# Kernel optimization log

Hardware: AMD Instinct MI355X
Metric: run time of the kernel (lower is better)

Reference implementation:

```python
import jax, jax.numpy as jnp
import numpy as np


def _maxpool2x2(x):
    # x: [B, C, H, W] -> [B, C, H//2, W//2]
    B, C, H, W = x.shape
    return x.reshape(B, C, H // 2, 2, W // 2, 2).max(axis=(3, 5))


def setup_inputs() -> dict:
    key = jax.random.key(0)
    ks = jax.random.split(key, 6)
    B, CH, H, W = 16, 128, 64, 64
    W_SCALE = 0.05  # keep pre-softmax logits in a sane range
    x = jax.random.normal(ks[0], (B, CH, H, W), dtype=jnp.float32)
    w_theta = jax.random.normal(ks[1], (CH // 8, CH), dtype=jnp.float32) * W_SCALE
    w_phi = jax.random.normal(ks[2], (CH // 8, CH), dtype=jnp.float32) * W_SCALE
    w_g = jax.random.normal(ks[3], (CH // 2, CH), dtype=jnp.float32) * W_SCALE
    w_o = jax.random.normal(ks[4], (CH, CH // 2), dtype=jnp.float32) * W_SCALE
    gamma = jax.random.normal(ks[5], (1,), dtype=jnp.float32)  # torch inits to 0; randomized for non-trivial output
    return {"x": x, "w_theta": w_theta, "w_phi": w_phi, "w_g": w_g, "w_o": w_o, "gamma": gamma}


def reference(x, w_theta, w_phi, w_g, w_o, gamma):
    B, C, H, W = x.shape
    N = H * W
    # 1x1 convs are channel GEMMs
    theta = jnp.einsum('oc,bchw->bohw', w_theta, x)          # [B, C/8, H, W]
    phi = _maxpool2x2(jnp.einsum('oc,bchw->bohw', w_phi, x))  # [B, C/8, H/2, W/2]
    g = _maxpool2x2(jnp.einsum('oc,bchw->bohw', w_g, x))      # [B, C/2, H/2, W/2]
    theta = theta.reshape(B, C // 8, N)        # [B, C/8, N]
    phi = phi.reshape(B, C // 8, N // 4)       # [B, C/8, N/4]
    g = g.reshape(B, C // 2, N // 4)           # [B, C/2, N/4]
    scores = jnp.einsum('bcn,bcm->bnm', theta, phi)  # [B, N, N/4]
    beta = jax.nn.softmax(scores, axis=-1)
    o = jnp.einsum('bcm,bnm->bcn', g, beta)          # [B, C/2, N]
    o = o.reshape(B, C // 2, H, W)
    o = jnp.einsum('oc,bchw->bohw', w_o, o)          # [B, C, H, W]
    return gamma[0] * o + x
```

## Files before the change

### kernel.cpp

```cpp
#include <hip/hip_runtime.h>
#include <hip/hip_bf16.h>


typedef __attribute__((ext_vector_type(8))) short bf16x8;
typedef __attribute__((ext_vector_type(16))) float f32x16;

#define LOG2E 1.4426950408889634f

__device__ __forceinline__ ushort f2bf(float f) {
    uint u = __float_as_uint(f);
    u += 0x7FFFu + ((u >> 16) & 1u);
    return (ushort)(u >> 16);
}
__device__ __forceinline__ uint pk2(float a, float b) {
    return (uint)f2bf(a) | ((uint)f2bf(b) << 16);
}
__device__ __forceinline__ uint pk2hw(float a, float b) {
    union { __hip_bfloat162 h; uint u; } cv;
    cv.h = __float22bfloat162_rn(make_float2(a, b));
    return cv.u;
}
__device__ __forceinline__ float exp2_hw(float v) {
    float r;
    asm("v_exp_f32 %0, %1" : "=v"(r) : "v"(v));
    return r;
}

__global__ __launch_bounds__(256) void k_convs(const float* __restrict__ x,
                                               const float* __restrict__ w_theta,
                                               const float* __restrict__ w_phi,
                                               const float* __restrict__ w_g,
                                               ushort* __restrict__ theta_b,
                                               ushort* __restrict__ phi_b,
                                               ushort* __restrict__ g_b) {
    __shared__ __align__(16) char smem[16384 + 32 * 72 * 2];
    const int tid = threadIdx.x;
    const int part = blockIdx.x >> 8;
    const int pb = blockIdx.x & 255;
    const int gq = pb * 64 + (tid >> 2);
    const int sub = tid & 3;
    const int b = gq >> 10, m = gq & 1023;
    const int h2 = m >> 5, w2 = m & 31;
    const int n = (2 * h2 + (sub >> 1)) * 64 + 2 * w2 + (sub & 1);
    const float* xp = x + (size_t)b * 128 * 4096 + n;

    if (part == 0) {
        float (*wt)[32] = (float (*)[32])smem;
        for (int i = tid; i < 2048; i += 256) { int o = i >> 7, c = i & 127; wt[c][o] = w_theta[i] * LOG2E; }
        for (int i = tid; i < 2048; i += 256) { int o = i >> 7, c = i & 127; wt[c][16 + o] = w_phi[i]; }
        __syncthreads();
        float th[16], ph[16];
#pragma unroll
        for (int o = 0; o < 16; ++o) { th[o] = 0.f; ph[o] = 0.f; }
        for (int c = 0; c < 128; ++c) {
            float xv = xp[(size_t)c * 4096];
            const float* wr = wt[c];
#pragma unroll
            for (int o = 0; o < 16; ++o) th[o] = fmaf(wr[o], xv, th[o]);
#pragma unroll
            for (int o = 0; o < 16; ++o) ph[o] = fmaf(wr[16 + o], xv, ph[o]);
        }
        uint4 t0, t1;
        t0.x = pk2(th[0], th[1]);  t0.y = pk2(th[2], th[3]);
        t0.z = pk2(th[4], th[5]);  t0.w = pk2(th[6], th[7]);
        t1.x = pk2(th[8], th[9]);  t1.y = pk2(th[10], th[11]);
        t1.z = pk2(th[12], th[13]); t1.w = pk2(th[14], th[15]);
        uint4* tp = (uint4*)(theta_b + ((size_t)b * 4096 + n) * 16);
        tp[0] = t0; tp[1] = t1;
#pragma unroll
        for (int o = 0; o < 16; ++o) {
            ph[o] = fmaxf(ph[o], __shfl_xor(ph[o], 1));
            ph[o] = fmaxf(ph[o], __shfl_xor(ph[o], 2));
        }
        if (sub == 0) {
            uint4 p0, p1;
            p0.x = pk2(ph[0], ph[1]);  p0.y = pk2(ph[2], ph[3]);
            p0.z = pk2(ph[4], ph[5]);  p0.w = pk2(ph[6], ph[7]);
            p1.x = pk2(ph[8], ph[9]);  p1.y = pk2(ph[10], ph[11]);
            p1.z = pk2(ph[12], ph[13]); p1.w = pk2(ph[14], ph[15]);
            uint4* pp = (uint4*)(phi_b + ((size_t)b * 1024 + m) * 16);
            pp[0] = p0; pp[1] = p1;
        }
    } else {
        const int gp = part - 1;
        float (*wg)[32] = (float (*)[32])smem;
        ushort (*gt)[72] = (ushort (*)[72])(smem + 16384);
        for (int i = tid; i < 4096; i += 256) { int o = i >> 7, c = i & 127; wg[c][o] = w_g[(gp * 32 + o) * 128 + c]; }
        __syncthreads();
        float gg[32];
#pragma unroll
        for (int o = 0; o < 32; ++o) gg[o] = 0.f;
        for (int c = 0; c < 128; ++c) {
            float xv = xp[(size_t)c * 4096];
            const float* wr = wg[c];
#pragma unroll
            for (int o = 0; o < 32; ++o) gg[o] = fmaf(wr[o], xv, gg[o]);
        }
#pragma unroll
        for (int o = 0; o < 32; ++o) {
            gg[o] = fmaxf(gg[o], __shfl_xor(gg[o], 1));
            gg[o] = fmaxf(gg[o], __shfl_xor(gg[o], 2));
        }
        const int col = tid >> 2;
#pragma unroll
        for (int cc = 0; cc < 8; ++cc) gt[8 * sub + cc][col] = f2bf(gg[8 * sub + cc]);
        __syncthreads();
        const int cl = tid >> 3, q = tid & 7;
        uint4 v = *(const uint4*)&gt[cl][8 * q];
        const int bb = pb >> 4, mb = (pb & 15) * 64;
        *(uint4*)(g_b + ((size_t)bb * 64 + gp * 32 + cl) * 1024 + mb + 8 * q) = v;
    }
}

__global__ __launch_bounds__(256) void k_attn(const ushort* __restrict__ theta_b,
                                              const ushort* __restrict__ phi_b,
                                              const ushort* __restrict__ g_b,
                                              const float* __restrict__ w_o,
                                              const float* __restrict__ x,
                                              const float* __restrict__ gamma,
                                              float* __restrict__ out) {
    const int tid = threadIdx.x;
    const int wave = tid >> 6, lane = tid & 63;
    const int l31 = lane & 31, h = lane >> 5;
    const int b = blockIdx.x >> 5, nt = blockIdx.x & 31;
    const int n = nt * 128 + wave * 32 + l31;

    bf16x8 thf = *(const bf16x8*)(theta_b + ((size_t)b * 4096 + n) * 16 + h * 8);

    const ushort* pbase = phi_b + (size_t)b * 1024 * 16 + h * 8;
    const ushort* gbase = g_b + ((size_t)b * 64 + l31) * 1024 + 8 * h;

    f32x16 o0 = {0,0,0,0,0,0,0,0,0,0,0,0,0,0,0,0};
    f32x16 o1 = {0,0,0,0,0,0,0,0,0,0,0,0,0,0,0,0};
    float sm0 = 0.f, sm1 = 0.f;

    bf16x8 phf = *(const bf16x8*)(pbase + (size_t)l31 * 16);
    bf16x8 gA0 = *(const bf16x8*)(gbase);
    bf16x8 gA1 = *(const bf16x8*)(gbase + 32 * 1024);
    bf16x8 gB0 = *(const bf16x8*)(gbase + 16);
    bf16x8 gB1 = *(const bf16x8*)(gbase + 16 + 32 * 1024);

    for (int mt = 0; mt < 32; ++mt) {
        const int m1 = ((mt + 1) & 31) * 32;
        bf16x8 nphf = *(const bf16x8*)(pbase + (size_t)(m1 + l31) * 16);
        bf16x8 ngA0 = *(const bf16x8*)(gbase + m1);
        bf16x8 ngA1 = *(const bf16x8*)(gbase + m1 + 32 * 1024);
        bf16x8 ngB0 = *(const bf16x8*)(gbase + m1 + 16);
        bf16x8 ngB1 = *(const bf16x8*)(gbase + m1 + 16 + 32 * 1024);

        f32x16 S = {0,0,0,0,0,0,0,0,0,0,0,0,0,0,0,0};
        S = __builtin_amdgcn_mfma_f32_32x32x16_bf16(phf, thf, S, 0, 0, 0);
        float p[16];
#pragma unroll
        for (int jj = 0; jj < 16; ++jj) p[jj] = exp2_hw(S[jj]);
        sm0 += ((p[0] + p[1]) + (p[2] + p[3])) + ((p[4] + p[5]) + (p[6] + p[7]));
        sm1 += ((p[8] + p[9]) + (p[10] + p[11])) + ((p[12] + p[13]) + (p[14] + p[15]));

        uint c0 = pk2hw(p[0], p[1]),   c1 = pk2hw(p[2], p[3]);
        uint c2 = pk2hw(p[4], p[5]),   c3 = pk2hw(p[6], p[7]);
        uint c4 = pk2hw(p[8], p[9]),   c5 = pk2hw(p[10], p[11]);
        uint c6 = pk2hw(p[12], p[13]), c7 = pk2hw(p[14], p[15]);
        uint q0 = (uint)__shfl_xor((int)(h ? c0 : c2), 32);
        uint q1 = (uint)__shfl_xor((int)(h ? c1 : c3), 32);
        uint q2 = (uint)__shfl_xor((int)(h ? c4 : c6), 32);
        uint q3 = (uint)__shfl_xor((int)(h ? c5 : c7), 32);
        union { bf16x8 v; uint u[4]; } B0, B1;
        if (h == 0) {
            B0.u[0] = c0; B0.u[1] = c1; B0.u[2] = q0; B0.u[3] = q1;
            B1.u[0] = c4; B1.u[1] = c5; B1.u[2] = q2; B1.u[3] = q3;
        } else {
            B0.u[0] = q0; B0.u[1] = q1; B0.u[2] = c2; B0.u[3] = c3;
            B1.u[0] = q2; B1.u[1] = q3; B1.u[2] = c6; B1.u[3] = c7;
        }
        o0 = __builtin_amdgcn_mfma_f32_32x32x16_bf16(gA0, B0.v, o0, 0, 0, 0);
        o1 = __builtin_amdgcn_mfma_f32_32x32x16_bf16(gA1, B0.v, o1, 0, 0, 0);
        o0 = __builtin_amdgcn_mfma_f32_32x32x16_bf16(gB0, B1.v, o0, 0, 0, 0);
        o1 = __builtin_amdgcn_mfma_f32_32x32x16_bf16(gB1, B1.v, o1, 0, 0, 0);

        phf = nphf; gA0 = ngA0; gA1 = ngA1; gB0 = ngB0; gB1 = ngB1;
    }
    float sm = sm0 + sm1;
    sm += __shfl_xor(sm, 32);
    const float inv = 1.f / sm;
#pragma unroll
    for (int jj = 0; jj < 16; ++jj) { o0[jj] *= inv; o1[jj] *= inv; }

    bf16x8 Bf[4];
#pragma unroll
    for (int kc = 0; kc < 4; ++kc) {
        const f32x16& oo = (kc < 2) ? o0 : o1;
        const int base = 8 * (kc & 1);
        uint Pa0 = pk2(oo[base + 0], oo[base + 1]);
        uint Pa1 = pk2(oo[base + 2], oo[base + 3]);
        uint Pb0 = pk2(oo[base + 4], oo[base + 5]);
        uint Pb1 = pk2(oo[base + 6], oo[base + 7]);
        uint z0 = h ? Pa0 : Pb0, z1 = h ? Pa1 : Pb1;
        uint r0 = (uint)__shfl_xor((int)z0, 32);
        uint r1 = (uint)__shfl_xor((int)z1, 32);
        union { bf16x8 v; uint u[4]; } Bx;
        if (h == 0) { Bx.u[0] = Pa0; Bx.u[1] = Pa1; Bx.u[2] = r0;  Bx.u[3] = r1; }
        else        { Bx.u[0] = r0;  Bx.u[1] = r1;  Bx.u[2] = Pb0; Bx.u[3] = Pb1; }
        Bf[kc] = Bx.v;
    }

    const float gm = gamma[0];
#pragma unroll
    for (int cof = 0; cof < 4; ++cof) {
        f32x16 oc = {0,0,0,0,0,0,0,0,0,0,0,0,0,0,0,0};
#pragma unroll
        for (int kc = 0; kc < 4; ++kc) {
            const float* wp = w_o + (32 * cof + l31) * 64 + 16 * kc + 8 * h;
            float4 wa = *(const float4*)(wp);
            float4 wb = *(const float4*)(wp + 4);
            union { bf16x8 v; uint u[4]; } W;
            W.u[0] = pk2(wa.x, wa.y); W.u[1] = pk2(wa.z, wa.w);
            W.u[2] = pk2(wb.x, wb.y); W.u[3] = pk2(wb.z, wb.w);
            oc = __builtin_amdgcn_mfma_f32_32x32x16_bf16(W.v, Bf[kc], oc, 0, 0, 0);
        }
#pragma unroll
        for (int jj = 0; jj < 16; ++jj) {
            int co = 32 * cof + (jj & 3) + 8 * (jj >> 2) + 4 * h;
            size_t idx = ((size_t)(b * 128 + co)) * 4096 + n;
            out[idx] = fmaf(gm, oc[jj], x[idx]);
        }
    }
}

extern "C" void kernel_launch(void* const* d_in, const int* in_sizes, int n_in,
                              void* d_out, int out_size, void* d_ws, size_t ws_size,
                              hipStream_t stream) {
    const float* x       = (const float*)d_in[0];
    const float* w_theta = (const float*)d_in[1];
    const float* w_phi   = (const float*)d_in[2];
    const float* w_g     = (const float*)d_in[3];
    const float* w_o     = (const float*)d_in[4];
    const float* gamma   = (const float*)d_in[5];
    float* out = (float*)d_out;

    ushort* theta_b = (ushort*)d_ws;
    ushort* phi_b   = theta_b + 1048576;
    ushort* g_b     = phi_b + 262144;

    k_convs<<<768, 256, 0, stream>>>(x, w_theta, w_phi, w_g, theta_b, phi_b, g_b);
    k_attn<<<512, 256, 0, stream>>>(theta_b, phi_b, g_b, w_o, x, gamma, out);
}
```

Baseline: 162.5 us.

## Use MFMA for projection convs and stage phi/g tiles through LDS in attention

The conv kernel is rewritten so each block stages a bf16, XOR-swizzled x tile and packed bf16 weight fragments in LDS, then computes theta, phi and g with MFMA instead of scalar FMA loops. It also fuses all three projections into one block type, cutting the grid from 768 to 512 blocks and removing the redundant reads of x across parts. The attention kernel now loads phi/g fragments cooperatively into a double-buffered LDS ring shared across the four waves, instead of each wave fetching them from global memory. The cost is bf16 rounding of x and the weights before the projections, more LDS use, and a block barrier per group of four key tiles.

After: 146.1 us. -10.1%, faster.

```diff
diff --git a/kernel.cpp b/kernel.cpp
--- a/kernel.cpp
+++ b/kernel.cpp
@@ -33,82 +33,115 @@
                                                ushort* __restrict__ theta_b,
                                                ushort* __restrict__ phi_b,
                                                ushort* __restrict__ g_b) {
-    __shared__ __align__(16) char smem[16384 + 32 * 72 * 2];
+    __shared__ uint  xl[8192];
+    __shared__ uint4 wl[1536];
     const int tid = threadIdx.x;
-    const int part = blockIdx.x >> 8;
-    const int pb = blockIdx.x & 255;
-    const int gq = pb * 64 + (tid >> 2);
-    const int sub = tid & 3;
-    const int b = gq >> 10, m = gq & 1023;
-    const int h2 = m >> 5, w2 = m & 31;
-    const int n = (2 * h2 + (sub >> 1)) * 64 + 2 * w2 + (sub & 1);
-    const float* xp = x + (size_t)b * 128 * 4096 + n;
-
-    if (part == 0) {
-        float (*wt)[32] = (float (*)[32])smem;
-        for (int i = tid; i < 2048; i += 256) { int o = i >> 7, c = i & 127; wt[c][o] = w_theta[i] * LOG2E; }
-        for (int i = tid; i < 2048; i += 256) { int o = i >> 7, c = i & 127; wt[c][16 + o] = w_phi[i]; }
-        __syncthreads();
-        float th[16], ph[16];
-#pragma unroll
-        for (int o = 0; o < 16; ++o) { th[o] = 0.f; ph[o] = 0.f; }
-        for (int c = 0; c < 128; ++c) {
-            float xv = xp[(size_t)c * 4096];
-            const float* wr = wt[c];
-#pragma unroll
-            for (int o = 0; o < 16; ++o) th[o] = fmaf(wr[o], xv, th[o]);
-#pragma unroll
-            for (int o = 0; o < 16; ++o) ph[o] = fmaf(wr[16 + o], xv, ph[o]);
-        }
-        uint4 t0, t1;
-        t0.x = pk2(th[0], th[1]);  t0.y = pk2(th[2], th[3]);
-        t0.z = pk2(th[4], th[5]);  t0.w = pk2(th[6], th[7]);
-        t1.x = pk2(th[8], th[9]);  t1.y = pk2(th[10], th[11]);
-        t1.z = pk2(th[12], th[13]); t1.w = pk2(th[14], th[15]);
-        uint4* tp = (uint4*)(theta_b + ((size_t)b * 4096 + n) * 16);
-        tp[0] = t0; tp[1] = t1;
-#pragma unroll
-        for (int o = 0; o < 16; ++o) {
-            ph[o] = fmaxf(ph[o], __shfl_xor(ph[o], 1));
-            ph[o] = fmaxf(ph[o], __shfl_xor(ph[o], 2));
-        }
-        if (sub == 0) {
-            uint4 p0, p1;
-            p0.x = pk2(ph[0], ph[1]);  p0.y = pk2(ph[2], ph[3]);
-            p0.z = pk2(ph[4], ph[5]);  p0.w = pk2(ph[6], ph[7]);
-            p1.x = pk2(ph[8], ph[9]);  p1.y = pk2(ph[10], ph[11]);
-            p1.z = pk2(ph[12], ph[13]); p1.w = pk2(ph[14], ph[15]);
-            uint4* pp = (uint4*)(phi_b + ((size_t)b * 1024 + m) * 16);
-            pp[0] = p0; pp[1] = p1;
-        }
-    } else {
-        const int gp = part - 1;
-        float (*wg)[32] = (float (*)[32])smem;
-        ushort (*gt)[72] = (ushort (*)[72])(smem + 16384);
-        for (int i = tid; i < 4096; i += 256) { int o = i >> 7, c = i & 127; wg[c][o] = w_g[(gp * 32 + o) * 128 + c]; }
-        __syncthreads();
-        float gg[32];
-#pragma unroll
-        for (int o = 0; o < 32; ++o) gg[o] = 0.f;
-        for (int c = 0; c < 128; ++c) {
-            float xv = xp[(size_t)c * 4096];
-            const float* wr = wg[c];
-#pragma unroll
-            for (int o = 0; o < 32; ++o) gg[o] = fmaf(wr[o], xv, gg[o]);
-        }
-#pragma unroll
-        for (int o = 0; o < 32; ++o) {
-            gg[o] = fmaxf(gg[o], __shfl_xor(gg[o], 1));
-            gg[o] = fmaxf(gg[o], __shfl_xor(gg[o], 2));
-        }
-        const int col = tid >> 2;
-#pragma unroll
-        for (int cc = 0; cc < 8; ++cc) gt[8 * sub + cc][col] = f2bf(gg[8 * sub + cc]);
-        __syncthreads();
-        const int cl = tid >> 3, q = tid & 7;
-        uint4 v = *(const uint4*)&gt[cl][8 * q];
-        const int bb = pb >> 4, mb = (pb & 15) * 64;
-        *(uint4*)(g_b + ((size_t)bb * 64 + gp * 32 + cl) * 1024 + mb + 8 * q) = v;
+    const int b = blockIdx.x >> 5, h2 = blockIdx.x & 31;
+    const int p0 = h2 * 128;
+
+    {
+        const int cp = tid & 63, pg = tid >> 6;
+        const float* r0 = x + ((size_t)(b * 128 + 2 * cp)) * 4096 + p0 + pg * 32;
+        const float4* v0 = (const float4*)r0;
+        const float4* v1 = (const float4*)(r0 + 4096);
+#pragma unroll
+        for (int j = 0; j < 8; ++j) {
+            float4 a = v0[j], c = v1[j];
+            const float* af = (const float*)&a;
+            const float* cf = (const float*)&c;
+#pragma unroll
+            for (int e = 0; e < 4; ++e) {
+                int pix = pg * 32 + 4 * j + e;
+                uint u = pk2hw(af[e], cf[e]);
+                int byt = (pix * 256 + cp * 4) ^ ((pix & 15) << 4);
+                xl[byt >> 2] = u;
+            }
+        }
+    }
+#pragma unroll
+    for (int i = 0; i < 6; ++i) {
+        int fi = tid + 256 * i;
+        int ln = fi & 63, sk = fi >> 6;
+        int s = sk >> 3, kc = sk & 7;
+        int r31 = ln & 31, rh = ln >> 5;
+        int c0 = kc * 16 + rh * 8;
+        const float* wr;
+        float scale = 1.0f;
+        if (s == 0) {
+            if (r31 < 16) { wr = w_theta + r31 * 128 + c0; scale = LOG2E; }
+            else          { wr = w_phi + (r31 - 16) * 128 + c0; }
+        } else if (s == 1) { wr = w_g + r31 * 128 + c0; }
+        else               { wr = w_g + (r31 + 32) * 128 + c0; }
+        float4 wa = *(const float4*)wr, wb = *(const float4*)(wr + 4);
+        uint4 fr;
+        fr.x = pk2hw(wa.x * scale, wa.y * scale);
+        fr.y = pk2hw(wa.z * scale, wa.w * scale);
+        fr.z = pk2hw(wb.x * scale, wb.y * scale);
+        fr.w = pk2hw(wb.z * scale, wb.w * scale);
+        wl[fi] = fr;
+    }
+    __syncthreads();
+
+    const int lane = tid & 63, wv = tid >> 6;
+    const int l31 = lane & 31, hh = lane >> 5;
+    const int sub = l31 & 3, q = wv * 8 + (l31 >> 2);
+    const int pix = 64 * (sub >> 1) + 2 * q + (sub & 1);
+    f32x16 a0 = {0,0,0,0,0,0,0,0,0,0,0,0,0,0,0,0};
+    f32x16 a1 = {0,0,0,0,0,0,0,0,0,0,0,0,0,0,0,0};
+    f32x16 a2 = {0,0,0,0,0,0,0,0,0,0,0,0,0,0,0,0};
+#pragma unroll
+    for (int kc = 0; kc < 8; ++kc) {
+        int byt = (pix * 256 + 32 * kc + 16 * hh) ^ ((pix & 15) << 4);
+        bf16x8 xf = *(const bf16x8*)((const char*)xl + byt);
+        bf16x8 w0 = *(const bf16x8*)&wl[(0 * 8 + kc) * 64 + lane];
+        bf16x8 w1 = *(const bf16x8*)&wl[(1 * 8 + kc) * 64 + lane];
+        bf16x8 w2 = *(const bf16x8*)&wl[(2 * 8 + kc) * 64 + lane];
+        a0 = __builtin_amdgcn_mfma_f32_32x32x16_bf16(w0, xf, a0, 0, 0, 0);
+        a1 = __builtin_amdgcn_mfma_f32_32x32x16_bf16(w1, xf, a1, 0, 0, 0);
+        a2 = __builtin_amdgcn_mfma_f32_32x32x16_bf16(w2, xf, a2, 0, 0, 0);
+    }
+
+    {
+        const int n = h2 * 128 + pix;
+        ushort* tp = theta_b + ((size_t)b * 4096 + n) * 16;
+        uint2 t0, t1;
+        t0.x = pk2hw(a0[0], a0[1]); t0.y = pk2hw(a0[2], a0[3]);
+        t1.x = pk2hw(a0[4], a0[5]); t1.y = pk2hw(a0[6], a0[7]);
+        *(uint2*)(tp + 4 * hh) = t0;
+        *(uint2*)(tp + 8 + 4 * hh) = t1;
+    }
+    float ph[8], g0[16], g1[16];
+#pragma unroll
+    for (int jj = 0; jj < 8; ++jj) ph[jj] = a0[8 + jj];
+#pragma unroll
+    for (int jj = 0; jj < 16; ++jj) { g0[jj] = a1[jj]; g1[jj] = a2[jj]; }
+#pragma unroll
+    for (int jj = 0; jj < 8; ++jj) {
+        ph[jj] = fmaxf(ph[jj], __shfl_xor(ph[jj], 1));
+        ph[jj] = fmaxf(ph[jj], __shfl_xor(ph[jj], 2));
+    }
+#pragma unroll
+    for (int jj = 0; jj < 16; ++jj) {
+        g0[jj] = fmaxf(g0[jj], __shfl_xor(g0[jj], 1));
+        g0[jj] = fmaxf(g0[jj], __shfl_xor(g0[jj], 2));
+        g1[jj] = fmaxf(g1[jj], __shfl_xor(g1[jj], 1));
+        g1[jj] = fmaxf(g1[jj], __shfl_xor(g1[jj], 2));
+    }
+    if (sub == 0) {
+        const int m = h2 * 32 + q;
+        ushort* pp = phi_b + ((size_t)b * 1024 + m) * 16;
+        uint2 p0v, p1v;
+        p0v.x = pk2hw(ph[0], ph[1]); p0v.y = pk2hw(ph[2], ph[3]);
+        p1v.x = pk2hw(ph[4], ph[5]); p1v.y = pk2hw(ph[6], ph[7]);
+        *(uint2*)(pp + 4 * hh) = p0v;
+        *(uint2*)(pp + 8 + 4 * hh) = p1v;
+        ushort* gp = g_b + (size_t)b * 64 * 1024 + m;
+#pragma unroll
+        for (int jj = 0; jj < 16; ++jj) {
+            int oc = (jj & 3) + 8 * (jj >> 2) + 4 * hh;
+            gp[(size_t)oc * 1024] = f2bf(g0[jj]);
+            gp[(size_t)(oc + 32) * 1024] = f2bf(g1[jj]);
+        }
     }
 }
 
@@ -119,6 +152,7 @@
                                               const float* __restrict__ x,
                                               const float* __restrict__ gamma,
                                               float* __restrict__ out) {
+    __shared__ uint4 sbuf[2][20][64];
     const int tid = threadIdx.x;
     const int wave = tid >> 6, lane = tid & 63;
     const int l31 = lane & 31, h = lane >> 5;
@@ -127,58 +161,85 @@
 
     bf16x8 thf = *(const bf16x8*)(theta_b + ((size_t)b * 4096 + n) * 16 + h * 8);
 
-    const ushort* pbase = phi_b + (size_t)b * 1024 * 16 + h * 8;
-    const ushort* gbase = g_b + ((size_t)b * 64 + l31) * 1024 + 8 * h;
+    const ushort* sp[5];
+    int sstep[5];
+#pragma unroll
+    for (int i = 0; i < 5; ++i) {
+        int mtLf = (tid >> 6) + 4 * i;
+        int mtL = mtLf / 5, f = mtLf % 5;
+        int m0 = mtL * 32;
+        if (f == 0) {
+            sp[i] = phi_b + ((size_t)b * 1024 + m0 + l31) * 16 + 8 * h;
+            sstep[i] = 128 * 16;
+        } else {
+            int off = (f >= 3 ? 16 : 0) + ((f == 2 || f == 4) ? 32 * 1024 : 0);
+            sp[i] = g_b + ((size_t)b * 64 + l31) * 1024 + m0 + 8 * h + off;
+            sstep[i] = 128;
+        }
+    }
+
+    uint4 stg[5];
+#pragma unroll
+    for (int i = 0; i < 5; ++i) { stg[i] = *(const uint4*)sp[i]; sp[i] += sstep[i]; }
+#pragma unroll
+    for (int i = 0; i < 5; ++i) sbuf[0][(tid >> 6) + 4 * i][lane] = stg[i];
+    __syncthreads();
 
     f32x16 o0 = {0,0,0,0,0,0,0,0,0,0,0,0,0,0,0,0};
     f32x16 o1 = {0,0,0,0,0,0,0,0,0,0,0,0,0,0,0,0};
     float sm0 = 0.f, sm1 = 0.f;
 
-    bf16x8 phf = *(const bf16x8*)(pbase + (size_t)l31 * 16);
-    bf16x8 gA0 = *(const bf16x8*)(gbase);
-    bf16x8 gA1 = *(const bf16x8*)(gbase + 32 * 1024);
-    bf16x8 gB0 = *(const bf16x8*)(gbase + 16);
-    bf16x8 gB1 = *(const bf16x8*)(gbase + 16 + 32 * 1024);
-
-    for (int mt = 0; mt < 32; ++mt) {
-        const int m1 = ((mt + 1) & 31) * 32;
-        bf16x8 nphf = *(const bf16x8*)(pbase + (size_t)(m1 + l31) * 16);
-        bf16x8 ngA0 = *(const bf16x8*)(gbase + m1);
-        bf16x8 ngA1 = *(const bf16x8*)(gbase + m1 + 32 * 1024);
-        bf16x8 ngB0 = *(const bf16x8*)(gbase + m1 + 16);
-        bf16x8 ngB1 = *(const bf16x8*)(gbase + m1 + 16 + 32 * 1024);
-
-        f32x16 S = {0,0,0,0,0,0,0,0,0,0,0,0,0,0,0,0};
-        S = __builtin_amdgcn_mfma_f32_32x32x16_bf16(phf, thf, S, 0, 0, 0);
-        float p[16];
-#pragma unroll
-        for (int jj = 0; jj < 16; ++jj) p[jj] = exp2_hw(S[jj]);
-        sm0 += ((p[0] + p[1]) + (p[2] + p[3])) + ((p[4] + p[5]) + (p[6] + p[7]));
-        sm1 += ((p[8] + p[9]) + (p[10] + p[11])) + ((p[12] + p[13]) + (p[14] + p[15]));
-
-        uint c0 = pk2hw(p[0], p[1]),   c1 = pk2hw(p[2], p[3]);
-        uint c2 = pk2hw(p[4], p[5]),   c3 = pk2hw(p[6], p[7]);
-        uint c4 = pk2hw(p[8], p[9]),   c5 = pk2hw(p[10], p[11]);
-        uint c6 = pk2hw(p[12], p[13]), c7 = pk2hw(p[14], p[15]);
-        uint q0 = (uint)__shfl_xor((int)(h ? c0 : c2), 32);
-        uint q1 = (uint)__shfl_xor((int)(h ? c1 : c3), 32);
-        uint q2 = (uint)__shfl_xor((int)(h ? c4 : c6), 32);
-        uint q3 = (uint)__shfl_xor((int)(h ? c5 : c7), 32);
-        union { bf16x8 v; uint u[4]; } B0, B1;
-        if (h == 0) {
-            B0.u[0] = c0; B0.u[1] = c1; B0.u[2] = q0; B0.u[3] = q1;
-            B1.u[0] = c4; B1.u[1] = c5; B1.u[2] = q2; B1.u[3] = q3;
-        } else {
-            B0.u[0] = q0; B0.u[1] = q1; B0.u[2] = c2; B0.u[3] = c3;
-            B1.u[0] = q2; B1.u[1] = q3; B1.u[2] = c6; B1.u[3] = c7;
-        }
-        o0 = __builtin_amdgcn_mfma_f32_32x32x16_bf16(gA0, B0.v, o0, 0, 0, 0);
-        o1 = __builtin_amdgcn_mfma_f32_32x32x16_bf16(gA1, B0.v, o1, 0, 0, 0);
-        o0 = __builtin_amdgcn_mfma_f32_32x32x16_bf16(gB0, B1.v, o0, 0, 0, 0);
-        o1 = __builtin_amdgcn_mfma_f32_32x32x16_bf16(gB1, B1.v, o1, 0, 0, 0);
-
-        phf = nphf; gA0 = ngA0; gA1 = ngA1; gB0 = ngB0; gB1 = ngB1;
-    }
+    for (int grp = 0; grp < 8; ++grp) {
+        const int cur = grp & 1;
+        if (grp < 7) {
+#pragma unroll
+            for (int i = 0; i < 5; ++i) { stg[i] = *(const uint4*)sp[i]; sp[i] += sstep[i]; }
+        }
+#pragma unroll
+        for (int mtL = 0; mtL < 4; ++mtL) {
+            const uint4* fr = &sbuf[cur][mtL * 5][0];
+            bf16x8 phf = *(const bf16x8*)&fr[0 * 64 + lane];
+            bf16x8 gA0 = *(const bf16x8*)&fr[1 * 64 + lane];
+            bf16x8 gA1 = *(const bf16x8*)&fr[2 * 64 + lane];
+            bf16x8 gB0 = *(const bf16x8*)&fr[3 * 64 + lane];
+            bf16x8 gB1 = *(const bf16x8*)&fr[4 * 64 + lane];
+
+            f32x16 S = {0,0,0,0,0,0,0,0,0,0,0,0,0,0,0,0};
+            S = __builtin_amdgcn_mfma_f32_32x32x16_bf16(phf, thf, S, 0, 0, 0);
+            float p[16];
+#pragma unroll
+            for (int jj = 0; jj < 16; ++jj) p[jj] = exp2_hw(S[jj]);
+            sm0 += ((p[0] + p[1]) + (p[2] + p[3])) + ((p[4] + p[5]) + (p[6] + p[7]));
+            sm1 += ((p[8] + p[9]) + (p[10] + p[11])) + ((p[12] + p[13]) + (p[14] + p[15]));
+
+            uint c0 = pk2hw(p[0], p[1]),   c1 = pk2hw(p[2], p[3]);
+            uint c2 = pk2hw(p[4], p[5]),   c3 = pk2hw(p[6], p[7]);
+            uint c4 = pk2hw(p[8], p[9]),   c5 = pk2hw(p[10], p[11]);
+            uint c6 = pk2hw(p[12], p[13]), c7 = pk2hw(p[14], p[15]);
+            uint q0 = (uint)__shfl_xor((int)(h ? c0 : c2), 32);
+            uint q1 = (uint)__shfl_xor((int)(h ? c1 : c3), 32);
+            uint q2 = (uint)__shfl_xor((int)(h ? c4 : c6), 32);
+            uint q3 = (uint)__shfl_xor((int)(h ? c5 : c7), 32);
+            union { bf16x8 v; uint u[4]; } B0, B1;
+            if (h == 0) {
+                B0.u[0] = c0; B0.u[1] = c1; B0.u[2] = q0; B0.u[3] = q1;
+                B1.u[0] = c4; B1.u[1] = c5; B1.u[2] = q2; B1.u[3] = q3;
+            } else {
+                B0.u[0] = q0; B0.u[1] = q1; B0.u[2] = c2; B0.u[3] = c3;
+                B1.u[0] = q2; B1.u[1] = q3; B1.u[2] = c6; B1.u[3] = c7;
+            }
+            o0 = __builtin_amdgcn_mfma_f32_32x32x16_bf16(gA0, B0.v, o0, 0, 0, 0);
+            o1 = __builtin_amdgcn_mfma_f32_32x32x16_bf16(gA1, B0.v, o1, 0, 0, 0);
+            o0 = __builtin_amdgcn_mfma_f32_32x32x16_bf16(gB0, B1.v, o0, 0, 0, 0);
+            o1 = __builtin_amdgcn_mfma_f32_32x32x16_bf16(gB1, B1.v, o1, 0, 0, 0);
+        }
+        if (grp < 7) {
+#pragma unroll
+            for (int i = 0; i < 5; ++i) sbuf[cur ^ 1][(tid >> 6) + 4 * i][lane] = stg[i];
+        }
+        __syncthreads();
+    }
+
     float sm = sm0 + sm1;
     sm += __shfl_xor(sm, 32);
     const float inv = 1.f / sm;
@@ -241,6 +302,6 @@
     ushort* phi_b   = theta_b + 1048576;
     ushort* g_b     = phi_b + 262144;
 
-    k_convs<<<768, 256, 0, stream>>>(x, w_theta, w_phi, w_g, theta_b, phi_b, g_b);
+    k_convs<<<512, 256, 0, stream>>>(x, w_theta, w_phi, w_g, theta_b, phi_b, g_b);
     k_attn<<<512, 256, 0, stream>>>(theta_b, phi_b, g_b, w_o, x, gamma, out);
 }
```
